# Kernel tuning notes

Hardware: AMD Instinct MI355X
Metric: run time of the kernel (lower is better)

Reference implementation:

```python
import jax, jax.numpy as jnp
import numpy as np

B, T, H, NH = 2, 2048, 1024, 16
HD = H // NH


def setup_inputs() -> dict:
    key = jax.random.key(0)
    ks = jax.random.split(key, 12)
    s = 1.0 / np.sqrt(H)
    inp = {
        "q": jax.random.normal(ks[0], (B, T, H), jnp.float32),
        "k": jax.random.normal(ks[1], (B, T, H), jnp.float32),
        "v": jax.random.normal(ks[2], (B, T, H), jnp.float32),
        "mask": jnp.tril(jnp.ones((T, T), jnp.int32))[None, None],  # causal [1,1,T,T]
        "w_q": jax.random.normal(ks[3], (H, H), jnp.float32) * s,
        "b_q": jax.random.normal(ks[4], (H,), jnp.float32) * 0.01,
        "w_k": jax.random.normal(ks[5], (H, H), jnp.float32) * s,
        "b_k": jax.random.normal(ks[6], (H,), jnp.float32) * 0.01,
        "w_v": jax.random.normal(ks[7], (H, H), jnp.float32) * s,
        "b_v": jax.random.normal(ks[8], (H,), jnp.float32) * 0.01,
        "w_o": jax.random.normal(ks[9], (H, H), jnp.float32) * s,
        "b_o": jax.random.normal(ks[10], (H,), jnp.float32) * 0.01,
    }
    return inp


def reference(q, k, v, mask, w_q, b_q, w_k, b_k, w_v, b_v, w_o, b_o):
    def split_heads(x):
        Bx, Tx, _ = x.shape
        return x.reshape(Bx, Tx, NH, HD).transpose(0, 2, 1, 3)  # [B,NH,T,HD]

    Q = split_heads(q @ w_q.T + b_q)
    K = split_heads(k @ w_k.T + b_k)
    V = split_heads(v @ w_v.T + b_v)

    scores = jnp.einsum("bhqd,bhkd->bhqk", Q, K) / np.sqrt(HD).astype(np.float32)
    scores = jnp.where(mask == 0, jnp.float32(-1e9), scores)
    weights = jax.nn.softmax(scores, axis=-1)  # dropout prob = 0.0
    out = jnp.einsum("bhqk,bhkd->bhqd", weights, V)
    out = out.transpose(0, 2, 1, 3).reshape(q.shape[0], q.shape[1], H)
    return out @ w_o.T + b_o
```

## Files before the change

### kernel.cpp

```cpp
#include <hip/hip_runtime.h>
#include <hip/hip_bf16.h>

#define Bb 2
#define Tt 2048
#define Hh 1024
#define NHh 16

typedef short bf16x8 __attribute__((ext_vector_type(8)));
typedef float f32x4 __attribute__((ext_vector_type(4)));
typedef unsigned short u16;
typedef unsigned int u32;
typedef u16 u16x4v __attribute__((ext_vector_type(4)));
typedef u32 u32x2v __attribute__((ext_vector_type(2)));

#define QK_SCALE 0.180336880f

#if __has_builtin(__builtin_amdgcn_exp2f)
__device__ __forceinline__ float exp2_fast(float x) { return __builtin_amdgcn_exp2f(x); }
#else
__device__ __forceinline__ float exp2_fast(float x) { return __expf(x * 0.69314718f); }
#endif

__device__ __forceinline__ u16 f2b(float x) {
  unsigned u = __builtin_bit_cast(unsigned, x);
  u += 0x7FFFu + ((u >> 16) & 1u);
  return (u16)(u >> 16);
}

__device__ __forceinline__ u32 cvt_pk(float lo, float hi) {
  u32 r;
  asm("v_cvt_pk_bf16_f32 %0, %1, %2" : "=v"(r) : "v"(lo), "v"(hi));
  return r;
}

__global__ __launch_bounds__(256) void cvt3_kernel(const float* __restrict__ s0,
                                                   const float* __restrict__ s1,
                                                   const float* __restrict__ s2,
                                                   u16* __restrict__ d0,
                                                   u16* __restrict__ d1,
                                                   u16* __restrict__ d2, int n4) {
  const int which = blockIdx.y;
  const float* src = which == 0 ? s0 : which == 1 ? s1 : s2;
  u16* dst = which == 0 ? d0 : which == 1 ? d1 : d2;
  int i = blockIdx.x * blockDim.x + threadIdx.x;
  int stride = gridDim.x * blockDim.x;
  for (; i < n4; i += stride) {
    float4 v = ((const float4*)src)[i];
    u16x4v o;
    o.x = f2b(v.x); o.y = f2b(v.y); o.z = f2b(v.z); o.w = f2b(v.w);
    ((u16x4v*)dst)[i] = o;
  }
}

__global__ __launch_bounds__(256) void cvt4_kernel(const float* __restrict__ s0,
                                                   const float* __restrict__ s1,
                                                   const float* __restrict__ s2,
                                                   const float* __restrict__ s3,
                                                   u16* __restrict__ d0,
                                                   u16* __restrict__ d1,
                                                   u16* __restrict__ d2,
                                                   u16* __restrict__ d3, int n4) {
  const int which = blockIdx.y;
  const float* src = which == 0 ? s0 : which == 1 ? s1 : which == 2 ? s2 : s3;
  u16* dst = which == 0 ? d0 : which == 1 ? d1 : which == 2 ? d2 : d3;
  const float sc = (which == 0) ? QK_SCALE : 1.0f;
  int i = blockIdx.x * blockDim.x + threadIdx.x;
  int stride = gridDim.x * blockDim.x;
  for (; i < n4; i += stride) {
    float4 v = ((const float4*)src)[i];
    u16x4v o;
    o.x = f2b(v.x * sc); o.y = f2b(v.y * sc); o.z = f2b(v.z * sc); o.w = f2b(v.w * sc);
    ((u16x4v*)dst)[i] = o;
  }
}

template<int NF, int MODE>
__device__ __forceinline__ void gemm_body(const u16* __restrict__ A,
                                          const u16* __restrict__ W,
                                          const float* __restrict__ bias, float bscale,
                                          void* __restrict__ Cout,
                                          u16* lA, u16* lB) {
  const int tid = threadIdx.x;
  const int lane = tid & 63;
  const int wid = tid >> 6;
  const int wr = wid >> 1, wc = wid & 1;
  const int g = lane >> 4, fr = lane & 15;
  const int mt = blockIdx.y, nt = blockIdx.x;
  constexpr int NT = NF * 32;

  f32x4 acc[4][NF];
#pragma unroll
  for (int m = 0; m < 4; ++m)
#pragma unroll
    for (int n = 0; n < NF; ++n) acc[m][n] = (f32x4){0.f, 0.f, 0.f, 0.f};

  const int srow = tid >> 3;
  const int scol = (tid & 7) * 8;

  bf16x8 ra[4], rb[NF];
#pragma unroll
  for (int ps = 0; ps < 4; ++ps)
    ra[ps] = *(const bf16x8*)(A + (size_t)(mt * 128 + ps * 32 + srow) * Hh + scol);
#pragma unroll
  for (int ps = 0; ps < NF; ++ps)
    rb[ps] = *(const bf16x8*)(W + (size_t)(nt * NT + ps * 32 + srow) * Hh + scol);
#pragma unroll
  for (int ps = 0; ps < 4; ++ps) {
    int r = ps * 32 + srow;
    *(bf16x8*)((char*)lA + r * 128 + ((scol * 2) ^ ((r & 7) << 4))) = ra[ps];
  }
#pragma unroll
  for (int ps = 0; ps < NF; ++ps) {
    int r = ps * 32 + srow;
    *(bf16x8*)((char*)lB + r * 128 + ((scol * 2) ^ ((r & 7) << 4))) = rb[ps];
  }
  __syncthreads();

  for (int kt = 0; kt < Hh; kt += 64) {
    if (kt + 64 < Hh) {
#pragma unroll
      for (int ps = 0; ps < 4; ++ps)
        ra[ps] = *(const bf16x8*)(A + (size_t)(mt * 128 + ps * 32 + srow) * Hh + kt + 64 + scol);
#pragma unroll
      for (int ps = 0; ps < NF; ++ps)
        rb[ps] = *(const bf16x8*)(W + (size_t)(nt * NT + ps * 32 + srow) * Hh + kt + 64 + scol);
    }
    bf16x8 af[4][2], bfv[NF][2];
#pragma unroll
    for (int m = 0; m < 4; ++m)
#pragma unroll
      for (int ks = 0; ks < 2; ++ks) {
        int r = wr * 64 + m * 16 + fr;
        af[m][ks] = *(const bf16x8*)((const char*)lA + r * 128 + ((ks * 64 + g * 16) ^ ((r & 7) << 4)));
      }
#pragma unroll
    for (int n = 0; n < NF; ++n)
#pragma unroll
      for (int ks = 0; ks < 2; ++ks) {
        int r = wc * (NT / 2) + n * 16 + fr;
        bfv[n][ks] = *(const bf16x8*)((const char*)lB + r * 128 + ((ks * 64 + g * 16) ^ ((r & 7) << 4)));
      }
#pragma unroll
    for (int m = 0; m < 4; ++m)
#pragma unroll
      for (int n = 0; n < NF; ++n)
#pragma unroll
        for (int ks = 0; ks < 2; ++ks)
          acc[m][n] = __builtin_amdgcn_mfma_f32_16x16x32_bf16(af[m][ks], bfv[n][ks],
                                                              acc[m][n], 0, 0, 0);
    if (kt + 64 < Hh) {
      __syncthreads();
#pragma unroll
      for (int ps = 0; ps < 4; ++ps) {
        int r = ps * 32 + srow;
        *(bf16x8*)((char*)lA + r * 128 + ((scol * 2) ^ ((r & 7) << 4))) = ra[ps];
      }
#pragma unroll
      for (int ps = 0; ps < NF; ++ps) {
        int r = ps * 32 + srow;
        *(bf16x8*)((char*)lB + r * 128 + ((scol * 2) ^ ((r & 7) << 4))) = rb[ps];
      }
      __syncthreads();
    }
  }

#pragma unroll
  for (int n = 0; n < NF; ++n) {
    int Cc = nt * NT + wc * (NT / 2) + n * 16 + fr;
    float bv = bias[Cc] * bscale;
#pragma unroll
    for (int m = 0; m < 4; ++m) {
#pragma unroll
      for (int j = 0; j < 4; ++j) {
        int R = mt * 128 + wr * 64 + m * 16 + g * 4 + j;
        float val = acc[m][n][j] + bv;
        if constexpr (MODE == 0) {
          int bb = R >> 11, t = R & (Tt - 1);
          int h = Cc >> 6, d = Cc & 63;
          ((u16*)Cout)[(((size_t)(bb * NHh + h) * Tt + t) << 6) + d] = f2b(val);
        } else if constexpr (MODE == 2) {
          int bb = R >> 11, t = R & (Tt - 1);
          int h = Cc >> 6, d = Cc & 63;
          ((u16*)Cout)[(((size_t)(bb * NHh + h) * 64 + d) << 11) + t] = f2b(val);
        } else {
          ((float*)Cout)[(size_t)R * Hh + Cc] = val;
        }
      }
    }
  }
}

__global__ __launch_bounds__(256, 3) void proj_qkv_kernel(
    const u16* __restrict__ qb, const u16* __restrict__ kb, const u16* __restrict__ vb,
    const u16* __restrict__ wqb, const u16* __restrict__ wkb, const u16* __restrict__ wvb,
    const float* __restrict__ biq, const float* __restrict__ bik, const float* __restrict__ biv,
    u16* __restrict__ Qp, u16* __restrict__ Kp, u16* __restrict__ Vt) {
  __shared__ u16 lA[128 * 64];
  __shared__ u16 lB[64 * 64];
  const int z = blockIdx.z;
  const u16* A = (z == 0) ? qb : (z == 1) ? kb : vb;
  const u16* W = (z == 0) ? wqb : (z == 1) ? wkb : wvb;
  const float* bi = (z == 0) ? biq : (z == 1) ? bik : biv;
  if (z == 2) gemm_body<2, 2>(A, W, bi, 1.0f, Vt, lA, lB);
  else if (z == 0) gemm_body<2, 0>(A, W, bi, QK_SCALE, Qp, lA, lB);
  else gemm_body<2, 0>(A, W, bi, 1.0f, Kp, lA, lB);
}

__global__ __launch_bounds__(256, 2) void gemm_out_kernel(
    const u16* __restrict__ A, const u16* __restrict__ W,
    const float* __restrict__ bias, float* __restrict__ Cout) {
  __shared__ u16 lA[128 * 64];
  __shared__ u16 lB[64 * 64];
  gemm_body<2, 1>(A, W, bias, 1.0f, Cout, lA, lB);
}

__global__ __launch_bounds__(256, 4) void attn_kernel(const u16* __restrict__ Qp,
                                                      const u16* __restrict__ Kp,
                                                      const u16* __restrict__ Vt,
                                                      u16* __restrict__ AO) {
  __shared__ u16 lK[2][64 * 64];
  __shared__ u16 lV[2][64 * 64];
  __shared__ u16 lP[64 * 64];
  const int tid = threadIdx.x;
  const int lane = tid & 63;
  const int w = tid >> 6;
  const int g = lane >> 4, fr = lane & 15;
  const int L = blockIdx.x;
  const int i = L & 255, k4 = L >> 8;
  const int bh = i & 31, s8 = i >> 5;
  const int t2 = s8 * 2 + (k4 >> 1);
  const int qt = (k4 & 1) ? (31 - t2) : t2;
  const int q0 = qt * 64;

  bf16x8 qf[2];
  {
    const u16* qrow = Qp + (((size_t)bh * Tt + q0 + w * 16 + fr) << 6) + g * 8;
    qf[0] = *(const bf16x8*)(qrow);
    qf[1] = *(const bf16x8*)(qrow + 32);
  }

  const int srow = tid >> 3;
  const int scol = (tid & 7) * 8;
  const int sswz = (scol * 2) ^ ((srow & 7) << 4);

  bf16x8 rk[2], rv[2];
#pragma unroll
  for (int ps = 0; ps < 2; ++ps) {
    rk[ps] = *(const bf16x8*)(Kp + (((size_t)bh * Tt + ps * 32 + srow) << 6) + scol);
    rv[ps] = *(const bf16x8*)(Vt + (((size_t)bh * 64 + ps * 32 + srow) << 11) + scol);
  }
#pragma unroll
  for (int ps = 0; ps < 2; ++ps) {
    *(bf16x8*)((char*)lK[0] + (ps * 32 + srow) * 128 + sswz) = rk[ps];
    *(bf16x8*)((char*)lV[0] + (ps * 32 + srow) * 128 + sswz) = rv[ps];
  }
  __syncthreads();

  float m_r = -1e30f, l_r = 0.f;
  f32x4 acc[4];
#pragma unroll
  for (int nd = 0; nd < 4; ++nd) acc[nd] = (f32x4){0.f, 0.f, 0.f, 0.f};

  const int prow = w * 16 + fr;
  const int psw = (prow & 7) << 4;
  const int qoff = w * 16 + fr;

  for (int jt = 0; jt <= qt; ++jt) {
    const char* bK = (const char*)lK[jt & 1];
    const char* bV = (const char*)lV[jt & 1];
    if (jt < qt) {
#pragma unroll
      for (int ps = 0; ps < 2; ++ps) {
        rk[ps] = *(const bf16x8*)(Kp + (((size_t)bh * Tt + (jt + 1) * 64 + ps * 32 + srow) << 6) + scol);
        rv[ps] = *(const bf16x8*)(Vt + (((size_t)bh * 64 + ps * 32 + srow) << 11) + (jt + 1) * 64 + scol);
      }
    }
    f32x4 s[4];
    __builtin_amdgcn_s_setprio(1);
#pragma unroll
    for (int n = 0; n < 4; ++n) {
      s[n] = (f32x4){0.f, 0.f, 0.f, 0.f};
      int rbase = (n * 16 + fr) * 128;
      int rsw = (fr & 7) << 4;
#pragma unroll
      for (int ks = 0; ks < 2; ++ks) {
        bf16x8 ak = *(const bf16x8*)(bK + rbase + ((ks * 64 + g * 16) ^ rsw));
        s[n] = __builtin_amdgcn_mfma_f32_16x16x32_bf16(ak, qf[ks], s[n], 0, 0, 0);
      }
    }
    __builtin_amdgcn_s_setprio(0);

    float tm = -1e30f;
    if (jt == qt) {
#pragma unroll
      for (int n = 0; n < 4; ++n)
#pragma unroll
        for (int r = 0; r < 4; ++r) {
          if (n * 16 + g * 4 + r > qoff) s[n][r] = -1e30f;
          tm = fmaxf(tm, s[n][r]);
        }
    } else {
#pragma unroll
      for (int n = 0; n < 4; ++n)
#pragma unroll
        for (int r = 0; r < 4; ++r) tm = fmaxf(tm, s[n][r]);
    }
    tm = fmaxf(tm, __shfl_xor(tm, 16));
    tm = fmaxf(tm, __shfl_xor(tm, 32));
    if (!__all(tm <= m_r + 8.0f)) {
      float mn = fmaxf(m_r, tm);
      float sc = exp2_fast(m_r - mn);
      m_r = mn;
      l_r *= sc;
      float scj[4];
#pragma unroll
      for (int j = 0; j < 4; ++j) scj[j] = __shfl(sc, g * 4 + j);
#pragma unroll
      for (int nd = 0; nd < 4; ++nd)
#pragma unroll
        for (int j = 0; j < 4; ++j) acc[nd][j] *= scj[j];
    }
    float rs = 0.f;
    u32 pw[4][2];
#pragma unroll
    for (int n = 0; n < 4; ++n) {
      float p0 = exp2_fast(s[n][0] - m_r);
      float p1 = exp2_fast(s[n][1] - m_r);
      float p2 = exp2_fast(s[n][2] - m_r);
      float p3 = exp2_fast(s[n][3] - m_r);
      rs += (p0 + p1) + (p2 + p3);
      pw[n][0] = cvt_pk(p0, p1);
      pw[n][1] = cvt_pk(p2, p3);
    }
    rs += __shfl_xor(rs, 16);
    rs += __shfl_xor(rs, 32);
    l_r += rs;
    bf16x8 pa[2];
    {
      char* base = (char*)lP + prow * 128;
#pragma unroll
      for (int n = 0; n < 4; ++n)
        *(u32x2v*)(base + ((32 * n + 8 * g) ^ psw)) = (u32x2v){pw[n][0], pw[n][1]};
#pragma unroll
      for (int ks = 0; ks < 2; ++ks)
        pa[ks] = *(const bf16x8*)(base + ((ks * 64 + g * 16) ^ psw));
    }
    __builtin_amdgcn_s_setprio(1);
#pragma unroll
    for (int nd = 0; nd < 4; ++nd) {
      int rbase = (nd * 16 + fr) * 128;
      int rsw = (fr & 7) << 4;
#pragma unroll
      for (int ks = 0; ks < 2; ++ks) {
        bf16x8 bv = *(const bf16x8*)(bV + rbase + ((ks * 64 + g * 16) ^ rsw));
        acc[nd] = __builtin_amdgcn_mfma_f32_16x16x32_bf16(pa[ks], bv, acc[nd], 0, 0, 0);
      }
    }
    __builtin_amdgcn_s_setprio(0);
    if (jt < qt) {
#pragma unroll
      for (int ps = 0; ps < 2; ++ps) {
        *(bf16x8*)((char*)lK[(jt + 1) & 1] + (ps * 32 + srow) * 128 + sswz) = rk[ps];
        *(bf16x8*)((char*)lV[(jt + 1) & 1] + (ps * 32 + srow) * 128 + sswz) = rv[ps];
      }
      __syncthreads();
    }
  }

  const int b = bh >> 4, hh = bh & 15;
  float lj[4];
#pragma unroll
  for (int j = 0; j < 4; ++j) lj[j] = __shfl(l_r, g * 4 + j);
#pragma unroll
  for (int j = 0; j < 4; ++j) {
    float inv = 1.0f / lj[j];
    int qq = q0 + w * 16 + g * 4 + j;
    size_t base = (((size_t)b * Tt + qq) << 10) + hh * 64;
#pragma unroll
    for (int nd = 0; nd < 4; ++nd)
      AO[base + nd * 16 + fr] = f2b(acc[nd][j] * inv);
  }
}

extern "C" void kernel_launch(void* const* d_in, const int* in_sizes, int n_in,
                              void* d_out, int out_size, void* d_ws, size_t ws_size,
                              hipStream_t stream) {
  const float* q   = (const float*)d_in[0];
  const float* k   = (const float*)d_in[1];
  const float* v   = (const float*)d_in[2];
  const float* wq  = (const float*)d_in[4];
  const float* bq  = (const float*)d_in[5];
  const float* wk  = (const float*)d_in[6];
  const float* bk  = (const float*)d_in[7];
  const float* wv  = (const float*)d_in[8];
  const float* bv  = (const float*)d_in[9];
  const float* wo  = (const float*)d_in[10];
  const float* bo  = (const float*)d_in[11];

  char* ws = (char*)d_ws;
  const size_t SZB = (size_t)Bb * Tt * Hh * 2;
  const size_t WB  = (size_t)Hh * Hh * 2;
  u16* qb  = (u16*)(ws);
  u16* kb  = (u16*)(ws + SZB);
  u16* vb  = (u16*)(ws + 2 * SZB);
  u16* wqb = (u16*)(ws + 3 * SZB);
  u16* wkb = (u16*)(ws + 3 * SZB + WB);
  u16* wvb = (u16*)(ws + 3 * SZB + 2 * WB);
  u16* wob = (u16*)(ws + 3 * SZB + 3 * WB);
  u16* Qp  = (u16*)(ws + 3 * SZB + 4 * WB);
  u16* Kp  = (u16*)(ws + 4 * SZB + 4 * WB);
  u16* Vt  = (u16*)(ws + 5 * SZB + 4 * WB);
  u16* AO  = qb;

  const int N4_IN = (Bb * Tt * Hh) / 4;
  const int N4_W  = (Hh * Hh) / 4;
  cvt3_kernel<<<dim3(512, 3), 256, 0, stream>>>(q, k, v, qb, kb, vb, N4_IN);
  cvt4_kernel<<<dim3(128, 4), 256, 0, stream>>>(wq, wk, wv, wo, wqb, wkb, wvb, wob, N4_W);

  proj_qkv_kernel<<<dim3(Hh / 64, (Bb * Tt) / 128, 3), 256, 0, stream>>>(
      qb, kb, vb, wqb, wkb, wvb, bq, bk, bv, Qp, Kp, Vt);

  attn_kernel<<<dim3(1024), 256, 0, stream>>>(Qp, Kp, Vt, AO);

  gemm_out_kernel<<<dim3(Hh / 64, (Bb * Tt) / 128), 256, 0, stream>>>(
      AO, wob, bo, (float*)d_out);
}
```

Baseline: 121.2 us.

## Fuse fp32-to-bf16 input conversion into QKV projection and remap tile ordering

Removes the separate conversion kernel for q/k/v activations. The QKV projection GEMM now loads fp32 rows directly and converts them to bf16 in registers before staging into LDS. Both GEMMs also switch to a 1D grid with a custom mapping that groups eight M tiles per N tile, which is meant to improve L2 reuse of the weights. The cost is that the projection reads twice as many bytes per A tile, and since each A tile is reused across 16 N tiles it gets re-read and re-converted for each one.

```diff
diff --git a/kernel.cpp b/kernel.cpp
--- a/kernel.cpp
+++ b/kernel.cpp
@@ -31,25 +31,6 @@
   u32 r;
   asm("v_cvt_pk_bf16_f32 %0, %1, %2" : "=v"(r) : "v"(lo), "v"(hi));
   return r;
-}
-
-__global__ __launch_bounds__(256) void cvt3_kernel(const float* __restrict__ s0,
-                                                   const float* __restrict__ s1,
-                                                   const float* __restrict__ s2,
-                                                   u16* __restrict__ d0,
-                                                   u16* __restrict__ d1,
-                                                   u16* __restrict__ d2, int n4) {
-  const int which = blockIdx.y;
-  const float* src = which == 0 ? s0 : which == 1 ? s1 : s2;
-  u16* dst = which == 0 ? d0 : which == 1 ? d1 : d2;
-  int i = blockIdx.x * blockDim.x + threadIdx.x;
-  int stride = gridDim.x * blockDim.x;
-  for (; i < n4; i += stride) {
-    float4 v = ((const float4*)src)[i];
-    u16x4v o;
-    o.x = f2b(v.x); o.y = f2b(v.y); o.z = f2b(v.z); o.w = f2b(v.w);
-    ((u16x4v*)dst)[i] = o;
-  }
 }
 
 __global__ __launch_bounds__(256) void cvt4_kernel(const float* __restrict__ s0,
@@ -74,18 +55,17 @@
   }
 }
 
-template<int NF, int MODE>
-__device__ __forceinline__ void gemm_body(const u16* __restrict__ A,
+template<int NF, int MODE, bool CVTA>
+__device__ __forceinline__ void gemm_body(const void* __restrict__ Av,
                                           const u16* __restrict__ W,
                                           const float* __restrict__ bias, float bscale,
                                           void* __restrict__ Cout,
-                                          u16* lA, u16* lB) {
+                                          u16* lA, u16* lB, int mt, int nt) {
   const int tid = threadIdx.x;
   const int lane = tid & 63;
   const int wid = tid >> 6;
   const int wr = wid >> 1, wc = wid & 1;
   const int g = lane >> 4, fr = lane & 15;
-  const int mt = blockIdx.y, nt = blockIdx.x;
   constexpr int NT = NF * 32;
 
   f32x4 acc[4][NF];
@@ -99,8 +79,21 @@
 
   bf16x8 ra[4], rb[NF];
 #pragma unroll
-  for (int ps = 0; ps < 4; ++ps)
-    ra[ps] = *(const bf16x8*)(A + (size_t)(mt * 128 + ps * 32 + srow) * Hh + scol);
+  for (int ps = 0; ps < 4; ++ps) {
+    size_t off = (size_t)(mt * 128 + ps * 32 + srow) * Hh + scol;
+    if constexpr (CVTA) {
+      float4 f0 = *(const float4*)((const float*)Av + off);
+      float4 f1 = *(const float4*)((const float*)Av + off + 4);
+      bf16x8 o;
+      o[0] = (short)f2b(f0.x); o[1] = (short)f2b(f0.y);
+      o[2] = (short)f2b(f0.z); o[3] = (short)f2b(f0.w);
+      o[4] = (short)f2b(f1.x); o[5] = (short)f2b(f1.y);
+      o[6] = (short)f2b(f1.z); o[7] = (short)f2b(f1.w);
+      ra[ps] = o;
+    } else {
+      ra[ps] = *(const bf16x8*)((const u16*)Av + off);
+    }
+  }
 #pragma unroll
   for (int ps = 0; ps < NF; ++ps)
     rb[ps] = *(const bf16x8*)(W + (size_t)(nt * NT + ps * 32 + srow) * Hh + scol);
@@ -119,8 +112,21 @@
   for (int kt = 0; kt < Hh; kt += 64) {
     if (kt + 64 < Hh) {
 #pragma unroll
-      for (int ps = 0; ps < 4; ++ps)
-        ra[ps] = *(const bf16x8*)(A + (size_t)(mt * 128 + ps * 32 + srow) * Hh + kt + 64 + scol);
+      for (int ps = 0; ps < 4; ++ps) {
+        size_t off = (size_t)(mt * 128 + ps * 32 + srow) * Hh + kt + 64 + scol;
+        if constexpr (CVTA) {
+          float4 f0 = *(const float4*)((const float*)Av + off);
+          float4 f1 = *(const float4*)((const float*)Av + off + 4);
+          bf16x8 o;
+          o[0] = (short)f2b(f0.x); o[1] = (short)f2b(f0.y);
+          o[2] = (short)f2b(f0.z); o[3] = (short)f2b(f0.w);
+          o[4] = (short)f2b(f1.x); o[5] = (short)f2b(f1.y);
+          o[6] = (short)f2b(f1.z); o[7] = (short)f2b(f1.w);
+          ra[ps] = o;
+        } else {
+          ra[ps] = *(const bf16x8*)((const u16*)Av + off);
+        }
+      }
 #pragma unroll
       for (int ps = 0; ps < NF; ++ps)
         rb[ps] = *(const bf16x8*)(W + (size_t)(nt * NT + ps * 32 + srow) * Hh + kt + 64 + scol);
@@ -191,19 +197,20 @@
 }
 
 __global__ __launch_bounds__(256, 3) void proj_qkv_kernel(
-    const u16* __restrict__ qb, const u16* __restrict__ kb, const u16* __restrict__ vb,
+    const float* __restrict__ q, const float* __restrict__ k, const float* __restrict__ v,
     const u16* __restrict__ wqb, const u16* __restrict__ wkb, const u16* __restrict__ wvb,
     const float* __restrict__ biq, const float* __restrict__ bik, const float* __restrict__ biv,
     u16* __restrict__ Qp, u16* __restrict__ Kp, u16* __restrict__ Vt) {
   __shared__ u16 lA[128 * 64];
   __shared__ u16 lB[64 * 64];
-  const int z = blockIdx.z;
-  const u16* A = (z == 0) ? qb : (z == 1) ? kb : vb;
-  const u16* W = (z == 0) ? wqb : (z == 1) ? wkb : wvb;
-  const float* bi = (z == 0) ? biq : (z == 1) ? bik : biv;
-  if (z == 2) gemm_body<2, 2>(A, W, bi, 1.0f, Vt, lA, lB);
-  else if (z == 0) gemm_body<2, 0>(A, W, bi, QK_SCALE, Qp, lA, lB);
-  else gemm_body<2, 0>(A, W, bi, 1.0f, Kp, lA, lB);
+  const int id = blockIdx.x;
+  const int j = id >> 3;
+  const int slot = (id & 7) + 8 * (j >> 4);
+  const int nt = j & 15;
+  const int z = slot >> 5, mt = slot & 31;
+  if (z == 0)      gemm_body<2, 0, true>(q, wqb, biq, QK_SCALE, Qp, lA, lB, mt, nt);
+  else if (z == 1) gemm_body<2, 0, true>(k, wkb, bik, 1.0f, Kp, lA, lB, mt, nt);
+  else             gemm_body<2, 2, true>(v, wvb, biv, 1.0f, Vt, lA, lB, mt, nt);
 }
 
 __global__ __launch_bounds__(256, 2) void gemm_out_kernel(
@@ -211,7 +218,11 @@
     const float* __restrict__ bias, float* __restrict__ Cout) {
   __shared__ u16 lA[128 * 64];
   __shared__ u16 lB[64 * 64];
-  gemm_body<2, 1>(A, W, bias, 1.0f, Cout, lA, lB);
+  const int id = blockIdx.x;
+  const int j = id >> 3;
+  const int mt = (id & 7) + 8 * (j >> 4);
+  const int nt = j & 15;
+  gemm_body<2, 1, false>(A, W, bias, 1.0f, Cout, lA, lB, mt, nt);
 }
 
 __global__ __launch_bounds__(256, 4) void attn_kernel(const u16* __restrict__ Qp,
@@ -400,28 +411,23 @@
   char* ws = (char*)d_ws;
   const size_t SZB = (size_t)Bb * Tt * Hh * 2;
   const size_t WB  = (size_t)Hh * Hh * 2;
-  u16* qb  = (u16*)(ws);
-  u16* kb  = (u16*)(ws + SZB);
-  u16* vb  = (u16*)(ws + 2 * SZB);
-  u16* wqb = (u16*)(ws + 3 * SZB);
-  u16* wkb = (u16*)(ws + 3 * SZB + WB);
-  u16* wvb = (u16*)(ws + 3 * SZB + 2 * WB);
-  u16* wob = (u16*)(ws + 3 * SZB + 3 * WB);
-  u16* Qp  = (u16*)(ws + 3 * SZB + 4 * WB);
-  u16* Kp  = (u16*)(ws + 4 * SZB + 4 * WB);
-  u16* Vt  = (u16*)(ws + 5 * SZB + 4 * WB);
-  u16* AO  = qb;
-
-  const int N4_IN = (Bb * Tt * Hh) / 4;
-  const int N4_W  = (Hh * Hh) / 4;
-  cvt3_kernel<<<dim3(512, 3), 256, 0, stream>>>(q, k, v, qb, kb, vb, N4_IN);
+  u16* wqb = (u16*)(ws);
+  u16* wkb = (u16*)(ws + WB);
+  u16* wvb = (u16*)(ws + 2 * WB);
+  u16* wob = (u16*)(ws + 3 * WB);
+  u16* Qp  = (u16*)(ws + 4 * WB);
+  u16* Kp  = (u16*)(ws + 4 * WB + SZB);
+  u16* Vt  = (u16*)(ws + 4 * WB + 2 * SZB);
+  u16* AO  = (u16*)(ws + 4 * WB + 3 * SZB);
+
+  const int N4_W = (Hh * Hh) / 4;
   cvt4_kernel<<<dim3(128, 4), 256, 0, stream>>>(wq, wk, wv, wo, wqb, wkb, wvb, wob, N4_W);
 
-  proj_qkv_kernel<<<dim3(Hh / 64, (Bb * Tt) / 128, 3), 256, 0, stream>>>(
-      qb, kb, vb, wqb, wkb, wvb, bq, bk, bv, Qp, Kp, Vt);
+  proj_qkv_kernel<<<dim3(1536), 256, 0, stream>>>(
+      q, k, v, wqb, wkb, wvb, bq, bk, bv, Qp, Kp, Vt);
 
   attn_kernel<<<dim3(1024), 256, 0, stream>>>(Qp, Kp, Vt, AO);
 
-  gemm_out_kernel<<<dim3(Hh / 64, (Bb * Tt) / 128), 256, 0, stream>>>(
+  gemm_out_kernel<<<dim3(512), 256, 0, stream>>>(
       AO, wob, bo, (float*)d_out);
 }
```

Result: faster. 118.8 us (-2.0%).
